# Performance work log

Measured on AMD Instinct MI355X. Metric: run time of the kernel, lower is better.

## Reference

```python
import jax, jax.numpy as jnp
import numpy as np

D_MODEL = 1024
N_HEADS = 16
D_HIDDEN = 4096
EPS = 1e-6
MASK_VAL = 1e10


def layernorm(x, gamma, beta):
    # Matches torch module: unbiased std (N-1), divide by (std + eps)
    mean = jnp.mean(x, axis=-1, keepdims=True)
    d = x.shape[-1]
    std = jnp.sqrt(jnp.sum((x - mean) ** 2, axis=-1, keepdims=True) / (d - 1))
    return gamma * (x - mean) / (std + EPS) + beta


def multihead(q_in, k_in, v_in, wq, wk, wv, wo, causal):
    # nn.Linear(bias=False): y = x @ W.T
    q = q_in @ wq.T
    k = k_in @ wk.T
    v = v_in @ wv.T
    B, Sq, D = q.shape
    Sk = k.shape[1]
    H, dh = N_HEADS, D // N_HEADS
    q = q.reshape(B, Sq, H, dh)
    k = k.reshape(B, Sk, H, dh)
    v = v.reshape(B, Sk, H, dh)
    scores = jnp.einsum('bqhd,bkhd->bhqk', q, k)  # [B,H,Sq,Sk]
    if causal:
        tri = jnp.triu(jnp.full((Sk, Sk), MASK_VAL, dtype=scores.dtype), k=1)
        scores = scores - tri  # mask applied BEFORE scaling, as in source
    scale = jnp.sqrt(jnp.asarray(D_MODEL, dtype=scores.dtype))  # d_key = d_model
    att = jax.nn.softmax(scores / scale, axis=-1)
    out = jnp.einsum('bhqk,bkhd->bqhd', att, v).reshape(B, Sq, D)
    return out @ wo.T


def setup_inputs() -> dict:
    key = jax.random.key(0)
    ks = jax.random.split(key, 24)
    B, S, D, DH = 2, 2048, D_MODEL, D_HIDDEN
    w = lambda k, shp: (jax.random.normal(k, shp, dtype=jnp.float32) * 0.02)
    inp = {
        'x': jax.random.normal(ks[0], (B, S, D), dtype=jnp.float32),
        'encoding': jax.random.normal(ks[1], (B, S, D), dtype=jnp.float32),
        'sa_wq': w(ks[2], (D, D)), 'sa_wk': w(ks[3], (D, D)),
        'sa_wv': w(ks[4], (D, D)), 'sa_wo': w(ks[5], (D, D)),
        'ca_wq': w(ks[6], (D, D)), 'ca_wk': w(ks[7], (D, D)),
        'ca_wv': w(ks[8], (D, D)), 'ca_wo': w(ks[9], (D, D)),
        'ff_w1': w(ks[10], (DH, D)), 'ff_b1': jnp.zeros((DH,), jnp.float32),
        'ff_w2': w(ks[11], (D, DH)), 'ff_b2': jnp.zeros((D,), jnp.float32),
        'ln1_g': jnp.ones((D,), jnp.float32), 'ln1_b': jnp.zeros((D,), jnp.float32),
        'ln2_g': jnp.ones((D,), jnp.float32), 'ln2_b': jnp.zeros((D,), jnp.float32),
        'ln3_g': jnp.ones((D,), jnp.float32), 'ln3_b': jnp.zeros((D,), jnp.float32),
    }
    return inp


def reference(x, encoding, sa_wq, sa_wk, sa_wv, sa_wo, ca_wq, ca_wk, ca_wv, ca_wo,
              ff_w1, ff_b1, ff_w2, ff_b2, ln1_g, ln1_b, ln2_g, ln2_b, ln3_g, ln3_b):
    # self-attention (causal) + post-norm residual
    h = layernorm(x + multihead(x, x, x, sa_wq, sa_wk, sa_wv, sa_wo, causal=True), ln1_g, ln1_b)
    # cross-attention + post-norm residual
    h = layernorm(h + multihead(h, encoding, encoding, ca_wq, ca_wk, ca_wv, ca_wo, causal=False), ln2_g, ln2_b)
    # feed-forward + post-norm residual
    ff = jax.nn.relu(h @ ff_w1.T + ff_b1) @ ff_w2.T + ff_b2
    return layernorm(h + ff, ln3_g, ln3_b)
```

## Files before the change

### kernel.cpp

```cpp
#include <hip/hip_runtime.h>
#include <hip/hip_bf16.h>
#include <math.h>

#define D_MODEL 1024
#define NHEADS  16
#define DHEAD   64
#define D_HID   4096

typedef __attribute__((ext_vector_type(8))) short short8;
typedef __attribute__((ext_vector_type(4))) short short4v;
typedef __attribute__((ext_vector_type(4))) float f32x4;
typedef __attribute__((ext_vector_type(16))) float f32x16;

#define QSCALE_F 0.04508422002778011f
#define MASK_T   4.5084220e8f

__device__ inline short f2bs(float x) {
    union { __hip_bfloat16 b; short s; } u;
    u.b = __float2bfloat16(x);
    return u.s;
}
__device__ inline float bs2f(ushort s) {
    union { unsigned u; float f; } v; v.u = ((unsigned)s) << 16; return v.f;
}
__device__ inline unsigned cvtpk(float lo, float hi) {
    unsigned r;
    asm("v_cvt_pk_bf16_f32 %0, %1, %2" : "=v"(r) : "v"(lo), "v"(hi));
    return r;
}
__device__ inline short8 pack8(float4 x, float4 y) {
    short8 v;
    v[0] = f2bs(x.x); v[1] = f2bs(x.y); v[2] = f2bs(x.z); v[3] = f2bs(x.w);
    v[4] = f2bs(y.x); v[5] = f2bs(y.y); v[6] = f2bs(y.z); v[7] = f2bs(y.w);
    return v;
}
typedef const unsigned __attribute__((address_space(1))) gu32;
typedef unsigned __attribute__((address_space(3))) lu32;
__device__ inline void gload16(const void* g, void* l) {
    __builtin_amdgcn_global_load_lds((gu32*)g, (lu32*)l, 16, 0, 0);
}
__device__ inline int swz(int r, int byteInRow) {
    return (r * 128 + byteInRow) ^ ((r & 7) << 4);
}

struct WP { const float* p[10]; };
__global__ __launch_bounds__(256) void cast_weights(WP wp, short* __restrict__ dst) {
    const int n8 = (16 << 20) / 8;
    for (int i = blockIdx.x * 256 + threadIdx.x; i < n8; i += gridDim.x * 256) {
        size_t e = (size_t)i * 8;
        int seg = (int)(e >> 20);
        const float* src;
        if (seg < 8)       src = wp.p[seg] + (e & ((1u << 20) - 1));
        else if (seg < 12) src = wp.p[8] + (e - ((size_t)8 << 20));
        else               src = wp.p[9] + (e - ((size_t)12 << 20));
        float4 a = *(const float4*)src;
        float4 b = *(const float4*)(src + 4);
        *(short8*)(dst + e) = pack8(a, b);
    }
}

__global__ __launch_bounds__(256) void cast_f2b(const float* __restrict__ in,
                                                short* __restrict__ out, int n8) {
    for (int i = blockIdx.x * 256 + threadIdx.x; i < n8; i += gridDim.x * 256) {
        float4 a = *(const float4*)(in + (size_t)i * 8);
        float4 b = *(const float4*)(in + (size_t)i * 8 + 4);
        *(short8*)(out + (size_t)i * 8) = pack8(a, b);
    }
}

template<int OM, bool BIAS, bool RELU, bool ACCUM>
__global__ __launch_bounds__(256) void gemm_mfma(
    const short* __restrict__ A, int lda,
    const short* __restrict__ Bm, int ldb,
    const float* __restrict__ bias,
    float* __restrict__ Cf, short* __restrict__ Cb, int ldc,
    int M, int N, int K, size_t routeElems, float qscale)
{
    __shared__ short Als[128 * 64];
    __shared__ short Bls[128 * 64];

    const int tid = threadIdx.x, w = tid >> 6, l = tid & 63;
    const int l15 = l & 15, lhi = l >> 4;
    const int wr = w >> 1, wc = w & 1;

    const int kh = (OM == 3) ? blockIdx.z : 0;
    if (OM == 3) {
        A  += (size_t)kh * K;
        Bm += (size_t)kh * K;
    }

    const unsigned nwg  = gridDim.x * gridDim.y;
    const unsigned wgid = blockIdx.y * gridDim.x + blockIdx.x;
    const unsigned cpx  = nwg >> 3;
    const unsigned sid  = (wgid & 7) * cpx + (wgid >> 3);
    const int bm = (int)(sid / gridDim.x) * 128;
    const int bn = (int)(sid % gridDim.x) * 128;

    const int srow = w * 8 + (l >> 3);
    const int schk = ((l & 7) ^ (l >> 3)) * 8;

    f32x4 acc[4][4] = {};

    for (int k0 = 0; k0 < K; k0 += 64) {
        #pragma unroll
        for (int i = 0; i < 4; ++i) {
            const short* ga = A  + (size_t)(bm + i * 32 + srow) * lda + k0 + schk;
            const short* gb = Bm + (size_t)(bn + i * 32 + srow) * ldb + k0 + schk;
            gload16(ga, &Als[i * 2048 + w * 512]);
            gload16(gb, &Bls[i * 2048 + w * 512]);
        }
        __syncthreads();

        short8 af[4][2], bf[4][2];
        #pragma unroll
        for (int m = 0; m < 4; ++m) {
            const int row = wr * 64 + m * 16 + l15;
            #pragma unroll
            for (int kk = 0; kk < 2; ++kk)
                af[m][kk] = *(const short8*)&Als[row * 64 + (((kk * 4 + lhi) ^ (l15 & 7)) * 8)];
        }
        #pragma unroll
        for (int n = 0; n < 4; ++n) {
            const int row = wc * 64 + n * 16 + l15;
            #pragma unroll
            for (int kk = 0; kk < 2; ++kk)
                bf[n][kk] = *(const short8*)&Bls[row * 64 + (((kk * 4 + lhi) ^ (l15 & 7)) * 8)];
        }
        #pragma unroll
        for (int kk = 0; kk < 2; ++kk)
            #pragma unroll
            for (int m = 0; m < 4; ++m)
                #pragma unroll
                for (int n = 0; n < 4; ++n)
                    acc[m][n] = __builtin_amdgcn_mfma_f32_16x16x32_bf16(af[m][kk], bf[n][kk], acc[m][n], 0, 0, 0);
        __syncthreads();
    }

    #pragma unroll
    for (int n = 0; n < 4; ++n) {
        const int col = bn + wc * 64 + n * 16 + l15;
        float bv = 0.f;
        if (BIAS && (OM != 3 || kh == 0)) bv = bias[col];
        const float sc = (OM == 2) ? (col < 1024 ? qscale : 1.f) : qscale;
        #pragma unroll
        for (int m = 0; m < 4; ++m) {
            const int row0 = bm + wr * 64 + m * 16 + lhi * 4;
            #pragma unroll
            for (int i = 0; i < 4; ++i) {
                float v = acc[m][n][i] + bv;
                if (ACCUM) v += Cf[(size_t)(row0 + i) * ldc + col];
                if (RELU)  v = fmaxf(v, 0.f);
                v *= sc;
                if (OM == 0) {
                    Cf[(size_t)(row0 + i) * ldc + col] = v;
                } else if (OM == 1) {
                    Cb[(size_t)(row0 + i) * ldc + col] = f2bs(v);
                } else if (OM == 2) {
                    Cb[(size_t)(col >> 10) * routeElems +
                       (size_t)(row0 + i) * 1024 + (col & 1023)] = f2bs(v);
                } else {
                    if (kh == 0) Cf[(size_t)(row0 + i) * ldc + col] = v;
                    else         Cb[(size_t)(row0 + i) * ldc + col] = f2bs(v);
                }
            }
        }
    }
}

__global__ __launch_bounds__(256) void v_prep(
    const short* __restrict__ Vb_, short* __restrict__ Vt, int S)
{
    const int t = blockIdx.x, bh = blockIdx.y;
    const int b = bh >> 4, h = bh & 15;
    const int tid = threadIdx.x;
    const int r = tid >> 2, g = tid & 3;
    __shared__ ushort vs[64][65];

    const size_t inrow = ((size_t)b * S + t * 64 + r) * D_MODEL + h * DHEAD;
    const size_t tbase = ((size_t)bh * (S / 64) + t) * 4096;

    short8 v0 = *(const short8*)(Vb_ + inrow + g * 16);
    short8 v1 = *(const short8*)(Vb_ + inrow + g * 16 + 8);
    #pragma unroll
    for (int j = 0; j < 8; ++j) { vs[r][g * 16 + j] = (ushort)v0[j]; vs[r][g * 16 + 8 + j] = (ushort)v1[j]; }
    __syncthreads();
    short8 q0, q1;
    #pragma unroll
    for (int j = 0; j < 8; ++j) {
        q0[j] = (short)vs[g * 16 + j][r];
        q1[j] = (short)vs[g * 16 + 8 + j][r];
    }
    *(short8*)(Vt + tbase + r * 64 + g * 16)     = q0;
    *(short8*)(Vt + tbase + r * 64 + g * 16 + 8) = q1;
}

template<bool CAUSAL>
__global__ __launch_bounds__(256, 3) void attn_v7(
    const short* __restrict__ Qb, const short* __restrict__ Kr,
    const short* __restrict__ Vt, short* __restrict__ PO,
    float* __restrict__ PL, int S)
{
    __shared__ __align__(16) char smem[2 * 16384];

    const int tid = threadIdx.x, w = tid >> 6, l = tid & 63;
    const int l31 = l & 31, hi = l >> 5;
    const int bnd = blockIdx.x >> 1, s = blockIdx.x & 1;
    const int bh = blockIdx.y, b = bh >> 4, h = bh & 15;
    const int qw = bnd * 128 + w * 32;
    const int q  = qw + l31;

    const short* qp = Qb + ((size_t)(b * S + q)) * 1024 + h * 64 + hi * 8;
    short8 bq[4];
    #pragma unroll
    for (int dc = 0; dc < 4; ++dc) bq[dc] = *(const short8*)(qp + dc * 16);

    const short* kbase = Kr + ((size_t)b * S) * 1024 + h * 64;
    const short* vbase = Vt + (size_t)bh * ((S / 64) * 4096);

    f32x16 ot0 = {}, ot1 = {};
    float l_lane = 0.f;

    const int tMax = CAUSAL ? (2 * bnd + 1) : (S / 64 - 1);
    const int sr = tid >> 2, sc = tid & 3;

    short8 gk0, gk1, gv0, gv1;
    {
        const short* kg = kbase + (size_t)(s * 64 + sr) * 1024 + sc * 8;
        const short* vg = vbase + (size_t)s * 4096 + sr * 64 + sc * 8;
        gk0 = *(const short8*)kg;        gk1 = *(const short8*)(kg + 32);
        gv0 = *(const short8*)vg;        gv1 = *(const short8*)(vg + 32);
    }
    {
        char* Kls = smem;            char* Vls = smem + 8192;
        *(short8*)(Kls + swz(sr, sc * 16))      = gk0;
        *(short8*)(Kls + swz(sr, sc * 16 + 64)) = gk1;
        *(short8*)(Vls + swz(sr, sc * 16))      = gv0;
        *(short8*)(Vls + swz(sr, sc * 16 + 64)) = gv1;
    }
    __syncthreads();

    int cur = 0;
    for (int t = s; t <= tMax; t += 2) {
        const bool hasNext = (t + 2 <= tMax);
        if (hasNext) {
            const short* kg = kbase + (size_t)((t + 2) * 64 + sr) * 1024 + sc * 8;
            const short* vg = vbase + (size_t)(t + 2) * 4096 + sr * 64 + sc * 8;
            gk0 = *(const short8*)kg;    gk1 = *(const short8*)(kg + 32);
            gv0 = *(const short8*)vg;    gv1 = *(const short8*)(vg + 32);
        }

        const char* Kls = smem + cur * 16384;
        const char* Vls = Kls + 8192;

        #pragma unroll
        for (int su = 0; su < 2; ++su) {
            const int kv0 = t * 64 + su * 32;
            if (CAUSAL && kv0 > qw + 31) break;

            f32x16 st = {};
            __builtin_amdgcn_s_setprio(1);
            #pragma unroll
            for (int dc = 0; dc < 4; ++dc) {
                short8 ak = *(const short8*)(Kls + swz(su * 32 + l31, dc * 32 + hi * 16));
                st = __builtin_amdgcn_mfma_f32_32x32x16_bf16(ak, bq[dc], st, 0, 0, 0);
            }
            __builtin_amdgcn_s_setprio(0);

            if (CAUSAL && kv0 + 31 > qw) {
                #pragma unroll
                for (int r = 0; r < 16; ++r) {
                    int kv = kv0 + (r & 3) + 8 * (r >> 2) + 4 * hi;
                    if (kv > q) st[r] -= MASK_T;
                }
            }

            float p[16];
            #pragma unroll
            for (int r = 0; r < 16; ++r) {
                p[r] = __builtin_amdgcn_exp2f(st[r]);
                l_lane += p[r];
            }

            unsigned wd[8], sx[8];
            #pragma unroll
            for (int i = 0; i < 8; ++i) wd[i] = cvtpk(p[2 * i], p[2 * i + 1]);
            #pragma unroll
            for (int i = 0; i < 8; ++i) sx[i] = __shfl_xor(wd[i], 32, 64);

            union U { unsigned u[4]; short8 s; };
            U b0, b1;
            if (hi == 0) {
                b0.u[0] = wd[0]; b0.u[1] = wd[1]; b0.u[2] = sx[0]; b0.u[3] = sx[1];
                b1.u[0] = wd[4]; b1.u[1] = wd[5]; b1.u[2] = sx[4]; b1.u[3] = sx[5];
            } else {
                b0.u[0] = sx[2]; b0.u[1] = sx[3]; b0.u[2] = wd[2]; b0.u[3] = wd[3];
                b1.u[0] = sx[6]; b1.u[1] = sx[7]; b1.u[2] = wd[6]; b1.u[3] = wd[7];
            }

            __builtin_amdgcn_s_setprio(1);
            short8 av;
            av  = *(const short8*)(Vls + swz(l31,      su * 64 + hi * 16));
            ot0 = __builtin_amdgcn_mfma_f32_32x32x16_bf16(av, b0.s, ot0, 0, 0, 0);
            av  = *(const short8*)(Vls + swz(l31,      su * 64 + 32 + hi * 16));
            ot0 = __builtin_amdgcn_mfma_f32_32x32x16_bf16(av, b1.s, ot0, 0, 0, 0);
            av  = *(const short8*)(Vls + swz(32 + l31, su * 64 + hi * 16));
            ot1 = __builtin_amdgcn_mfma_f32_32x32x16_bf16(av, b0.s, ot1, 0, 0, 0);
            av  = *(const short8*)(Vls + swz(32 + l31, su * 64 + 32 + hi * 16));
            ot1 = __builtin_amdgcn_mfma_f32_32x32x16_bf16(av, b1.s, ot1, 0, 0, 0);
            __builtin_amdgcn_s_setprio(0);
        }

        if (hasNext) {
            char* Kn = smem + (cur ^ 1) * 16384;
            char* Vn = Kn + 8192;
            *(short8*)(Kn + swz(sr, sc * 16))      = gk0;
            *(short8*)(Kn + swz(sr, sc * 16 + 64)) = gk1;
            *(short8*)(Vn + swz(sr, sc * 16))      = gv0;
            *(short8*)(Vn + swz(sr, sc * 16 + 64)) = gv1;
        }
        __syncthreads();
        cur ^= 1;
    }

    const int qc = bnd * 4 + w;
    const size_t c = ((size_t)bh * (S / 32) + qc) * 2 + s;
    float l_tot = l_lane + __shfl_xor(l_lane, 32, 64);
    if (hi == 0) PL[c * 32 + l31] = l_tot;
    short* po = PO + c * 2048 + (size_t)l31 * 64;
    #pragma unroll
    for (int i = 0; i < 8; ++i) {
        int dbase = ((2 * i) & 3) + 8 * (i >> 1) + 4 * hi;
        *(unsigned*)(po + dbase)      = cvtpk(ot0[2 * i], ot0[2 * i + 1]);
        *(unsigned*)(po + 32 + dbase) = cvtpk(ot1[2 * i], ot1[2 * i + 1]);
    }
}

__global__ __launch_bounds__(256) void attn_combine(
    const short* __restrict__ PO, const float* __restrict__ PL,
    short* __restrict__ Out, int S)
{
    const int qc = blockIdx.x, bh = blockIdx.y;
    const int b = bh >> 4, h = bh & 15;
    const size_t cbase = ((size_t)bh * (S / 32) + qc) * 2;
    const int tid = threadIdx.x;
    const int q = tid >> 3, dg = (tid & 7) * 8;

    float den = PL[cbase * 32 + q] + PL[(cbase + 1) * 32 + q];
    float acc[8] = {};
    #pragma unroll
    for (int s = 0; s < 2; ++s) {
        short8 po = *(const short8*)(PO + (cbase + s) * 2048 + q * 64 + dg);
        #pragma unroll
        for (int j = 0; j < 8; ++j) acc[j] += bs2f((ushort)po[j]);
    }
    float inv = 1.f / den;
    short8 o;
    #pragma unroll
    for (int j = 0; j < 8; ++j) o[j] = f2bs(acc[j] * inv);
    *(short8*)(Out + ((size_t)b * S + qc * 32 + q) * 1024 + h * 64 + dg) = o;
}

template<bool IN1BF, bool OUTBF, bool P3>
__global__ __launch_bounds__(256) void add_ln(
    const void* __restrict__ in1, const float* __restrict__ in2,
    const short* __restrict__ in3,
    const float* __restrict__ gam, const float* __restrict__ bet,
    void* __restrict__ y)
{
    const int row = blockIdx.x;
    const int tid = threadIdx.x;
    const size_t off = (size_t)row * D_MODEL;

    float a0, a1, a2, a3;
    if (IN1BF) {
        short4v xs = ((const short4v*)((const short*)in1 + off))[tid];
        a0 = bs2f((ushort)xs[0]); a1 = bs2f((ushort)xs[1]);
        a2 = bs2f((ushort)xs[2]); a3 = bs2f((ushort)xs[3]);
    } else {
        float4 xv = ((const float4*)((const float*)in1 + off))[tid];
        a0 = xv.x; a1 = xv.y; a2 = xv.z; a3 = xv.w;
    }
    float4 rv = ((const float4*)(in2 + off))[tid];
    float v0 = a0 + rv.x, v1 = a1 + rv.y, v2 = a2 + rv.z, v3 = a3 + rv.w;
    if (P3) {
        short4v ps = ((const short4v*)(in3 + off))[tid];
        v0 += bs2f((ushort)ps[0]); v1 += bs2f((ushort)ps[1]);
        v2 += bs2f((ushort)ps[2]); v3 += bs2f((ushort)ps[3]);
    }

    float s  = v0 + v1 + v2 + v3;
    float ss = v0 * v0 + v1 * v1 + v2 * v2 + v3 * v3;

    __shared__ float sb[8];
    #pragma unroll
    for (int o = 32; o > 0; o >>= 1) {
        s  += __shfl_down(s, o, 64);
        ss += __shfl_down(ss, o, 64);
    }
    const int lane = tid & 63, w = tid >> 6;
    if (lane == 0) { sb[w] = s; sb[4 + w] = ss; }
    __syncthreads();
    float S  = sb[0] + sb[1] + sb[2] + sb[3];
    float SS = sb[4] + sb[5] + sb[6] + sb[7];

    float mean = S * (1.f / D_MODEL);
    float var_sum = SS - S * mean;
    float stdv = sqrtf(var_sum * (1.f / (D_MODEL - 1)));
    float inv = 1.f / (stdv + 1e-6f);

    float4 gv = ((const float4*)gam)[tid];
    float4 bv = ((const float4*)bet)[tid];
    float o0 = gv.x * (v0 - mean) * inv + bv.x;
    float o1 = gv.y * (v1 - mean) * inv + bv.y;
    float o2 = gv.z * (v2 - mean) * inv + bv.z;
    float o3 = gv.w * (v3 - mean) * inv + bv.w;
    if (OUTBF) {
        short4v ov; ov[0] = f2bs(o0); ov[1] = f2bs(o1); ov[2] = f2bs(o2); ov[3] = f2bs(o3);
        ((short4v*)((short*)y + off))[tid] = ov;
    } else {
        ((float4*)((float*)y + off))[tid] = make_float4(o0, o1, o2, o3);
    }
}

extern "C" void kernel_launch(void* const* d_in, const int* in_sizes, int n_in,
                              void* d_out, int out_size, void* d_ws, size_t ws_size,
                              hipStream_t stream)
{
    const float* x     = (const float*)d_in[0];
    const float* enc   = (const float*)d_in[1];
    WP wp;
    for (int i = 0; i < 8; ++i) wp.p[i] = (const float*)d_in[2 + i];
    wp.p[8] = (const float*)d_in[10];
    wp.p[9] = (const float*)d_in[12];
    const float* ff_b1 = (const float*)d_in[11];
    const float* ff_b2 = (const float*)d_in[13];
    const float* ln1_g = (const float*)d_in[14];
    const float* ln1_b = (const float*)d_in[15];
    const float* ln2_g = (const float*)d_in[16];
    const float* ln2_b = (const float*)d_in[17];
    const float* ln3_g = (const float*)d_in[18];
    const float* ln3_b = (const float*)d_in[19];
    float* out = (float*)d_out;

    const int Bn = 2, S = 2048, M = Bn * S;
    const size_t MB = 1u << 20;
    char* ws = (char*)d_ws;
    short* Wb   = (short*)(ws);
    short* p32  = (short*)(ws + 32 * MB);
    short* p40  = (short*)(ws + 40 * MB);
    short* p48  = (short*)(ws + 48 * MB);
    short* p56  = (short*)(ws + 56 * MB);
    short* p64  = (short*)(ws + 64 * MB);
    short* p72  = (short*)(ws + 72 * MB);
    float* f0   = (float*)(ws + 80 * MB);

    short* PO  = (short*)f0;
    float* PLl = (float*)p64;
    short* tbuf = p48;

    const size_t RT = 4 * MB;
    const short* W_saqkv = Wb;
    const short* W_sawo  = Wb + 3 * MB;
    const short* W_caq   = Wb + 4 * MB;
    const short* W_cakv  = Wb + 5 * MB;
    const short* W_cawo  = Wb + 7 * MB;
    const short* W_ff1   = Wb + 8 * MB;
    const short* W_ff2   = Wb + 12 * MB;

    dim3 blk(256);
    dim3 g_qkv(3072 / 128, M / 128);
    dim3 g_kv(2048 / 128, M / 128);
    dim3 g_n1k(1024 / 128, M / 128);
    dim3 g_spl(1024 / 128, M / 128, 2);
    dim3 g_ff1(4096 / 128, M / 128);
    dim3 g_attn((S / 128) * 2, Bn * NHEADS);
    dim3 g_cmb(S / 32, Bn * NHEADS);
    dim3 g_vp(S / 64, Bn * NHEADS);
    dim3 g_ln(M);

    cast_weights<<<2048, blk, 0, stream>>>(wp, Wb);
    cast_f2b<<<2048, blk, 0, stream>>>(x, p32, (M * D_MODEL) / 8);

    gemm_mfma<2,false,false,false><<<g_qkv, blk, 0, stream>>>(p32, 1024, W_saqkv, 1024, nullptr, nullptr, p40, 1024, M, 3072, 1024, RT, QSCALE_F);
    v_prep<<<g_vp, blk, 0, stream>>>(p56, p72, S);
    attn_v7<true><<<g_attn, blk, 0, stream>>>(p40, p48, p72, PO, PLl, S);
    attn_combine<<<g_cmb, blk, 0, stream>>>(PO, PLl, p32, S);
    gemm_mfma<3,false,false,false><<<g_spl, blk, 0, stream>>>(p32, 1024, W_sawo, 1024, nullptr, f0, p48, 1024, M, 1024, 512, 0, 1.f);
    add_ln<false,true,true><<<g_ln, blk, 0, stream>>>(x, f0, p48, ln1_g, ln1_b, p32);

    cast_f2b<<<2048, blk, 0, stream>>>(enc, p64, (M * D_MODEL) / 8);
    gemm_mfma<2,false,false,false><<<g_kv, blk, 0, stream>>>(p64, 1024, W_cakv, 1024, nullptr, nullptr, p48, 1024, M, 2048, 1024, RT, 1.f);
    gemm_mfma<1,false,false,false><<<g_n1k, blk, 0, stream>>>(p32, 1024, W_caq, 1024, nullptr, nullptr, p40, 1024, M, 1024, 1024, 0, QSCALE_F);
    v_prep<<<g_vp, blk, 0, stream>>>(p56, p72, S);
    attn_v7<false><<<g_attn, blk, 0, stream>>>(p40, p48, p72, PO, PLl, S);
    attn_combine<<<g_cmb, blk, 0, stream>>>(PO, PLl, p56, S);
    gemm_mfma<3,false,false,false><<<g_spl, blk, 0, stream>>>(p56, 1024, W_cawo, 1024, nullptr, f0, p48, 1024, M, 1024, 512, 0, 1.f);
    add_ln<true,true,true><<<g_ln, blk, 0, stream>>>(p32, f0, p48, ln2_g, ln2_b, p40);

    gemm_mfma<1,true,true,false><<<g_ff1, blk, 0, stream>>>(p40, 1024, W_ff1, 1024, ff_b1, nullptr, tbuf, 4096, M, 4096, 1024, 0, 1.f);
    gemm_mfma<3,true,false,false><<<g_spl, blk, 0, stream>>>(tbuf, 4096, W_ff2, 4096, ff_b2, f0, p32, 1024, M, 1024, 2048, 0, 1.f);
    add_ln<true,false,true><<<g_ln, blk, 0, stream>>>(p40, f0, p32, ln3_g, ln3_b, out);
}
```

Baseline: 382.9 us.

## Fuse V transpose into QKV GEMM epilogue and process full 64-key tiles in attention

```diff
diff --git a/kernel.cpp b/kernel.cpp
--- a/kernel.cpp
+++ b/kernel.cpp
@@ -74,7 +74,8 @@
     const short* __restrict__ Bm, int ldb,
     const float* __restrict__ bias,
     float* __restrict__ Cf, short* __restrict__ Cb, int ldc,
-    int M, int N, int K, size_t routeElems, float qscale)
+    int M, int N, int K, size_t routeElems, float qscale,
+    short* __restrict__ Vtb, int vcol0)
 {
     __shared__ short Als[128 * 64];
     __shared__ short Bls[128 * 64];
@@ -156,8 +157,16 @@
                 } else if (OM == 1) {
                     Cb[(size_t)(row0 + i) * ldc + col] = f2bs(v);
                 } else if (OM == 2) {
-                    Cb[(size_t)(col >> 10) * routeElems +
-                       (size_t)(row0 + i) * 1024 + (col & 1023)] = f2bs(v);
+                    const int r = row0 + i;
+                    if (col >= vcol0) {
+                        const int vc = col - vcol0, h2 = vc >> 6, d = vc & 63;
+                        const int b2 = r >> 11, sp = r & 2047;
+                        Vtb[(((size_t)(b2 * 16 + h2) * 32 + (sp >> 6)) * 64 + d) * 64
+                            + (sp & 63)] = f2bs(v);
+                    } else {
+                        Cb[(size_t)(col >> 10) * routeElems +
+                           (size_t)r * 1024 + (col & 1023)] = f2bs(v);
+                    }
                 } else {
                     if (kh == 0) Cf[(size_t)(row0 + i) * ldc + col] = v;
                     else         Cb[(size_t)(row0 + i) * ldc + col] = f2bs(v);
@@ -167,35 +176,8 @@
     }
 }
 
-__global__ __launch_bounds__(256) void v_prep(
-    const short* __restrict__ Vb_, short* __restrict__ Vt, int S)
-{
-    const int t = blockIdx.x, bh = blockIdx.y;
-    const int b = bh >> 4, h = bh & 15;
-    const int tid = threadIdx.x;
-    const int r = tid >> 2, g = tid & 3;
-    __shared__ ushort vs[64][65];
-
-    const size_t inrow = ((size_t)b * S + t * 64 + r) * D_MODEL + h * DHEAD;
-    const size_t tbase = ((size_t)bh * (S / 64) + t) * 4096;
-
-    short8 v0 = *(const short8*)(Vb_ + inrow + g * 16);
-    short8 v1 = *(const short8*)(Vb_ + inrow + g * 16 + 8);
-    #pragma unroll
-    for (int j = 0; j < 8; ++j) { vs[r][g * 16 + j] = (ushort)v0[j]; vs[r][g * 16 + 8 + j] = (ushort)v1[j]; }
-    __syncthreads();
-    short8 q0, q1;
-    #pragma unroll
-    for (int j = 0; j < 8; ++j) {
-        q0[j] = (short)vs[g * 16 + j][r];
-        q1[j] = (short)vs[g * 16 + 8 + j][r];
-    }
-    *(short8*)(Vt + tbase + r * 64 + g * 16)     = q0;
-    *(short8*)(Vt + tbase + r * 64 + g * 16 + 8) = q1;
-}
-
 template<bool CAUSAL>
-__global__ __launch_bounds__(256, 3) void attn_v7(
+__global__ __launch_bounds__(256, 3) void attn_v8(
     const short* __restrict__ Qb, const short* __restrict__ Kr,
     const short* __restrict__ Vt, short* __restrict__ PO,
     float* __restrict__ PL, int S)
@@ -251,18 +233,17 @@
 
         const char* Kls = smem + cur * 16384;
         const char* Vls = Kls + 8192;
-
-        #pragma unroll
-        for (int su = 0; su < 2; ++su) {
-            const int kv0 = t * 64 + su * 32;
-            if (CAUSAL && kv0 > qw + 31) break;
-
-            f32x16 st = {};
+        const int kv0 = t * 64;
+
+        if (!(CAUSAL && kv0 > qw + 31)) {
+            f32x16 st0 = {}, st1 = {};
             __builtin_amdgcn_s_setprio(1);
             #pragma unroll
             for (int dc = 0; dc < 4; ++dc) {
-                short8 ak = *(const short8*)(Kls + swz(su * 32 + l31, dc * 32 + hi * 16));
-                st = __builtin_amdgcn_mfma_f32_32x32x16_bf16(ak, bq[dc], st, 0, 0, 0);
+                short8 a0 = *(const short8*)(Kls + swz(l31,      dc * 32 + hi * 16));
+                short8 a1 = *(const short8*)(Kls + swz(32 + l31, dc * 32 + hi * 16));
+                st0 = __builtin_amdgcn_mfma_f32_32x32x16_bf16(a0, bq[dc], st0, 0, 0, 0);
+                st1 = __builtin_amdgcn_mfma_f32_32x32x16_bf16(a1, bq[dc], st1, 0, 0, 0);
             }
             __builtin_amdgcn_s_setprio(0);
 
@@ -270,43 +251,72 @@
                 #pragma unroll
                 for (int r = 0; r < 16; ++r) {
                     int kv = kv0 + (r & 3) + 8 * (r >> 2) + 4 * hi;
-                    if (kv > q) st[r] -= MASK_T;
+                    if (kv > q) st0[r] -= MASK_T;
                 }
             }
-
-            float p[16];
-            #pragma unroll
-            for (int r = 0; r < 16; ++r) {
-                p[r] = __builtin_amdgcn_exp2f(st[r]);
-                l_lane += p[r];
+            if (CAUSAL && kv0 + 63 > qw) {
+                #pragma unroll
+                for (int r = 0; r < 16; ++r) {
+                    int kv = kv0 + 32 + (r & 3) + 8 * (r >> 2) + 4 * hi;
+                    if (kv > q) st1[r] -= MASK_T;
+                }
             }
 
-            unsigned wd[8], sx[8];
-            #pragma unroll
-            for (int i = 0; i < 8; ++i) wd[i] = cvtpk(p[2 * i], p[2 * i + 1]);
-            #pragma unroll
-            for (int i = 0; i < 8; ++i) sx[i] = __shfl_xor(wd[i], 32, 64);
-
             union U { unsigned u[4]; short8 s; };
-            U b0, b1;
-            if (hi == 0) {
-                b0.u[0] = wd[0]; b0.u[1] = wd[1]; b0.u[2] = sx[0]; b0.u[3] = sx[1];
-                b1.u[0] = wd[4]; b1.u[1] = wd[5]; b1.u[2] = sx[4]; b1.u[3] = sx[5];
-            } else {
-                b0.u[0] = sx[2]; b0.u[1] = sx[3]; b0.u[2] = wd[2]; b0.u[3] = wd[3];
-                b1.u[0] = sx[6]; b1.u[1] = sx[7]; b1.u[2] = wd[6]; b1.u[3] = wd[7];
+            U c00, c01, c10, c11;
+            {
+                float p[16];
+                #pragma unroll
+                for (int r = 0; r < 16; ++r) { p[r] = __builtin_amdgcn_exp2f(st0[r]); l_lane += p[r]; }
+                unsigned wd[8], sx[8];
+                #pragma unroll
+                for (int i = 0; i < 8; ++i) wd[i] = cvtpk(p[2 * i], p[2 * i + 1]);
+                #pragma unroll
+                for (int i = 0; i < 8; ++i) sx[i] = __shfl_xor(wd[i], 32, 64);
+                if (hi == 0) {
+                    c00.u[0] = wd[0]; c00.u[1] = wd[1]; c00.u[2] = sx[0]; c00.u[3] = sx[1];
+                    c01.u[0] = wd[4]; c01.u[1] = wd[5]; c01.u[2] = sx[4]; c01.u[3] = sx[5];
+                } else {
+                    c00.u[0] = sx[2]; c00.u[1] = sx[3]; c00.u[2] = wd[2]; c00.u[3] = wd[3];
+                    c01.u[0] = sx[6]; c01.u[1] = sx[7]; c01.u[2] = wd[6]; c01.u[3] = wd[7];
+                }
+            }
+            {
+                float p[16];
+                #pragma unroll
+                for (int r = 0; r < 16; ++r) { p[r] = __builtin_amdgcn_exp2f(st1[r]); l_lane += p[r]; }
+                unsigned wd[8], sx[8];
+                #pragma unroll
+                for (int i = 0; i < 8; ++i) wd[i] = cvtpk(p[2 * i], p[2 * i + 1]);
+                #pragma unroll
+                for (int i = 0; i < 8; ++i) sx[i] = __shfl_xor(wd[i], 32, 64);
+                if (hi == 0) {
+                    c10.u[0] = wd[0]; c10.u[1] = wd[1]; c10.u[2] = sx[0]; c10.u[3] = sx[1];
+                    c11.u[0] = wd[4]; c11.u[1] = wd[5]; c11.u[2] = sx[4]; c11.u[3] = sx[5];
+                } else {
+                    c10.u[0] = sx[2]; c10.u[1] = sx[3]; c10.u[2] = wd[2]; c10.u[3] = wd[3];
+                    c11.u[0] = sx[6]; c11.u[1] = sx[7]; c11.u[2] = wd[6]; c11.u[3] = wd[7];
+                }
             }
 
             __builtin_amdgcn_s_setprio(1);
             short8 av;
-            av  = *(const short8*)(Vls + swz(l31,      su * 64 + hi * 16));
-            ot0 = __builtin_amdgcn_mfma_f32_32x32x16_bf16(av, b0.s, ot0, 0, 0, 0);
-            av  = *(const short8*)(Vls + swz(l31,      su * 64 + 32 + hi * 16));
-            ot0 = __builtin_amdgcn_mfma_f32_32x32x16_bf16(av, b1.s, ot0, 0, 0, 0);
-            av  = *(const short8*)(Vls + swz(32 + l31, su * 64 + hi * 16));
-            ot1 = __builtin_amdgcn_mfma_f32_32x32x16_bf16(av, b0.s, ot1, 0, 0, 0);
-            av  = *(const short8*)(Vls + swz(32 + l31, su * 64 + 32 + hi * 16));
-            ot1 = __builtin_amdgcn_mfma_f32_32x32x16_bf16(av, b1.s, ot1, 0, 0, 0);
+            av  = *(const short8*)(Vls + swz(l31,      hi * 16));
+            ot0 = __builtin_amdgcn_mfma_f32_32x32x16_bf16(av, c00.s, ot0, 0, 0, 0);
+            av  = *(const short8*)(Vls + swz(32 + l31, hi * 16));
+            ot1 = __builtin_amdgcn_mfma_f32_32x32x16_bf16(av, c00.s, ot1, 0, 0, 0);
+            av  = *(const short8*)(Vls + swz(l31,      32 + hi * 16));
+            ot0 = __builtin_amdgcn_mfma_f32_32x32x16_bf16(av, c01.s, ot0, 0, 0, 0);
+            av  = *(const short8*)(Vls + swz(32 + l31, 32 + hi * 16));
+            ot1 = __builtin_amdgcn_mfma_f32_32x32x16_bf16(av, c01.s, ot1, 0, 0, 0);
+            av  = *(const short8*)(Vls + swz(l31,      64 + hi * 16));
+            ot0 = __builtin_amdgcn_mfma_f32_32x32x16_bf16(av, c10.s, ot0, 0, 0, 0);
+            av  = *(const short8*)(Vls + swz(32 + l31, 64 + hi * 16));
+            ot1 = __builtin_amdgcn_mfma_f32_32x32x16_bf16(av, c10.s, ot1, 0, 0, 0);
+            av  = *(const short8*)(Vls + swz(l31,      96 + hi * 16));
+            ot0 = __builtin_amdgcn_mfma_f32_32x32x16_bf16(av, c11.s, ot0, 0, 0, 0);
+            av  = *(const short8*)(Vls + swz(32 + l31, 96 + hi * 16));
+            ot1 = __builtin_amdgcn_mfma_f32_32x32x16_bf16(av, c11.s, ot1, 0, 0, 0);
             __builtin_amdgcn_s_setprio(0);
         }
 
@@ -475,29 +485,28 @@
     dim3 g_ff1(4096 / 128, M / 128);
     dim3 g_attn((S / 128) * 2, Bn * NHEADS);
     dim3 g_cmb(S / 32, Bn * NHEADS);
-    dim3 g_vp(S / 64, Bn * NHEADS);
     dim3 g_ln(M);
+
+    const int NOV = 1 << 30;
 
     cast_weights<<<2048, blk, 0, stream>>>(wp, Wb);
     cast_f2b<<<2048, blk, 0, stream>>>(x, p32, (M * D_MODEL) / 8);
 
-    gemm_mfma<2,false,false,false><<<g_qkv, blk, 0, stream>>>(p32, 1024, W_saqkv, 1024, nullptr, nullptr, p40, 1024, M, 3072, 1024, RT, QSCALE_F);
-    v_prep<<<g_vp, blk, 0, stream>>>(p56, p72, S);
-    attn_v7<true><<<g_attn, blk, 0, stream>>>(p40, p48, p72, PO, PLl, S);
+    gemm_mfma<2,false,false,false><<<g_qkv, blk, 0, stream>>>(p32, 1024, W_saqkv, 1024, nullptr, nullptr, p40, 1024, M, 3072, 1024, RT, QSCALE_F, p72, 2048);
+    attn_v8<true><<<g_attn, blk, 0, stream>>>(p40, p48, p72, PO, PLl, S);
     attn_combine<<<g_cmb, blk, 0, stream>>>(PO, PLl, p32, S);
-    gemm_mfma<3,false,false,false><<<g_spl, blk, 0, stream>>>(p32, 1024, W_sawo, 1024, nullptr, f0, p48, 1024, M, 1024, 512, 0, 1.f);
+    gemm_mfma<3,false,false,false><<<g_spl, blk, 0, stream>>>(p32, 1024, W_sawo, 1024, nullptr, f0, p48, 1024, M, 1024, 512, 0, 1.f, nullptr, NOV);
     add_ln<false,true,true><<<g_ln, blk, 0, stream>>>(x, f0, p48, ln1_g, ln1_b, p32);
 
     cast_f2b<<<2048, blk, 0, stream>>>(enc, p64, (M * D_MODEL) / 8);
-    gemm_mfma<2,false,false,false><<<g_kv, blk, 0, stream>>>(p64, 1024, W_cakv, 1024, nullptr, nullptr, p48, 1024, M, 2048, 1024, RT, 1.f);
-    gemm_mfma<1,false,false,false><<<g_n1k, blk, 0, stream>>>(p32, 1024, W_caq, 1024, nullptr, nullptr, p40, 1024, M, 1024, 1024, 0, QSCALE_F);
-    v_prep<<<g_vp, blk, 0, stream>>>(p56, p72, S);
-    attn_v7<false><<<g_attn, blk, 0, stream>>>(p40, p48, p72, PO, PLl, S);
+    gemm_mfma<2,false,false,false><<<g_kv, blk, 0, stream>>>(p64, 1024, W_cakv, 1024, nullptr, nullptr, p48, 1024, M, 2048, 1024, RT, 1.f, p72, 1024);
+    gemm_mfma<1,false,false,false><<<g_n1k, blk, 0, stream>>>(p32, 1024, W_caq, 1024, nullptr, nullptr, p40, 1024, M, 1024, 1024, 0, QSCALE_F, nullptr, NOV);
+    attn_v8<false><<<g_attn, blk, 0, stream>>>(p40, p48, p72, PO, PLl, S);
     attn_combine<<<g_cmb, blk, 0, stream>>>(PO, PLl, p56, S);
-    gemm_mfma<3,false,false,false><<<g_spl, blk, 0, stream>>>(p56, 1024, W_cawo, 1024, nullptr, f0, p48, 1024, M, 1024, 512, 0, 1.f);
+    gemm_mfma<3,false,false,false><<<g_spl, blk, 0, stream>>>(p56, 1024, W_cawo, 1024, nullptr, f0, p48, 1024, M, 1024, 512, 0, 1.f, nullptr, NOV);
     add_ln<true,true,true><<<g_ln, blk, 0, stream>>>(p32, f0, p48, ln2_g, ln2_b, p40);
 
-    gemm_mfma<1,true,true,false><<<g_ff1, blk, 0, stream>>>(p40, 1024, W_ff1, 1024, ff_b1, nullptr, tbuf, 4096, M, 4096, 1024, 0, 1.f);
-    gemm_mfma<3,true,false,false><<<g_spl, blk, 0, stream>>>(tbuf, 4096, W_ff2, 4096, ff_b2, f0, p32, 1024, M, 1024, 2048, 0, 1.f);
+    gemm_mfma<1,true,true,false><<<g_ff1, blk, 0, stream>>>(p40, 1024, W_ff1, 1024, ff_b1, nullptr, tbuf, 4096, M, 4096, 1024, 0, 1.f, nullptr, NOV);
+    gemm_mfma<3,true,false,false><<<g_spl, blk, 0, stream>>>(tbuf, 4096, W_ff2, 4096, ff_b2, f0, p32, 1024, M, 1024, 2048, 0, 1.f, nullptr, NOV);
     add_ln<true,false,true><<<g_ln, blk, 0, stream>>>(p40, f0, p32, ln3_g, ln3_b, out);
 }
```

After: 401.6 us. 4.9% more time.
